# Optimization experiments

Measured on AMD Instinct MI355X. Metric: run time of the kernel, lower is better.

Reference implementation:

```python
import jax, jax.numpy as jnp
import numpy as np


def setup_inputs() -> dict:
    key = jax.random.key(0)
    kq, kk, kv = jax.random.split(key, 3)
    B, H, S, D = 4, 12, 2048, 64
    query = jax.random.normal(kq, (B, H, S, D), dtype=jnp.float32)
    k = jax.random.normal(kk, (B, H, S, D), dtype=jnp.float32)
    value = jax.random.normal(kv, (B, H, S, D), dtype=jnp.float32)
    return {"query": query, "key": k, "value": value}


def reference(query, key, value):
    # scores = Q K^T / sqrt(d_k)  -> [B, H, S, S]
    d_k = query.shape[-1]
    scale = 1.0 / jnp.sqrt(jnp.asarray(d_k, dtype=query.dtype))
    scores = jnp.einsum('bhqd,bhkd->bhqk', query, key) * scale
    attention = jax.nn.softmax(scores, axis=-1)
    # dropout p=0.0 -> identity
    output = jnp.einsum('bhqk,bhkd->bhqd', attention, value)
    return (output, attention)
```

## Files before the change

kernel.cpp:

```cpp
#include <hip/hip_runtime.h>
#include <hip/hip_bf16.h>

typedef short bf16x8_t __attribute__((ext_vector_type(8)));
typedef float f32x4_t __attribute__((ext_vector_type(4)));

#define SDIM 2048
#define DDIM 64
#define KBLK 64
#define NIT  (SDIM / KBLK)
#define NBH  48

__device__ __forceinline__ unsigned short f2bf(float f) {
    return __builtin_bit_cast(unsigned short, (__bf16)f);
}
__device__ __forceinline__ unsigned int pack2(float lo, float hi) {
    return ((unsigned int)f2bf(hi) << 16) | (unsigned int)f2bf(lo);
}
__device__ __forceinline__ bf16x8_t pack8(f32x4_t a, f32x4_t b) {
    bf16x8_t r;
    r[0] = (short)f2bf(a[0]); r[1] = (short)f2bf(a[1]);
    r[2] = (short)f2bf(a[2]); r[3] = (short)f2bf(a[3]);
    r[4] = (short)f2bf(b[0]); r[5] = (short)f2bf(b[1]);
    r[6] = (short)f2bf(b[2]); r[7] = (short)f2bf(b[3]);
    return r;
}
__device__ __forceinline__ bf16x8_t pack8s(f32x4_t a, f32x4_t b, float s) {
    bf16x8_t r;
    r[0] = (short)f2bf(a[0] * s); r[1] = (short)f2bf(a[1] * s);
    r[2] = (short)f2bf(a[2] * s); r[3] = (short)f2bf(a[3] * s);
    r[4] = (short)f2bf(b[0] * s); r[5] = (short)f2bf(b[1] * s);
    r[6] = (short)f2bf(b[2] * s); r[7] = (short)f2bf(b[3] * s);
    return r;
}
struct uint4s { unsigned int x, y, z, w; };

__device__ __forceinline__ void lds_sync() {
    asm volatile("s_waitcnt lgkmcnt(0)" ::: "memory");
    __builtin_amdgcn_s_barrier();
    asm volatile("" ::: "memory");
}

__global__ __launch_bounds__(256) void cvt_k_kernel(const float* __restrict__ K,
                                                    unsigned short* __restrict__ Kb) {
    size_t i = ((size_t)blockIdx.x * 256 + threadIdx.x) * 8;
    f32x4_t a = *(const f32x4_t*)(K + i);
    f32x4_t b = *(const f32x4_t*)(K + i + 4);
    *(bf16x8_t*)(Kb + i) = pack8(a, b);
}

__global__ __launch_bounds__(256) void tr_v_kernel(const float* __restrict__ V,
                                                   unsigned short* __restrict__ VT) {
    __shared__ unsigned short lt[64 * 72];
    const int bh = blockIdx.x >> 5;
    const int kt = blockIdx.x & 31;
    const float* Vb = V + (size_t)bh * (SDIM * DDIM) + (size_t)kt * 64 * DDIM;
    unsigned short* VTb = VT + (size_t)bh * (DDIM * SDIM) + kt * 64;
    const int t = threadIdx.x;
    {
        const int kl = t >> 2, dg = t & 3;
        const float* vp = Vb + kl * DDIM + dg * 16;
        f32x4_t v0 = *(const f32x4_t*)vp;
        f32x4_t v1 = *(const f32x4_t*)(vp + 4);
        f32x4_t v2 = *(const f32x4_t*)(vp + 8);
        f32x4_t v3 = *(const f32x4_t*)(vp + 12);
#pragma unroll
        for (int j = 0; j < 16; ++j) {
            float f = (j < 4) ? v0[j] : (j < 8) ? v1[j - 4] : (j < 12) ? v2[j - 8] : v3[j - 12];
            lt[(dg * 16 + j) * 72 + kl] = f2bf(f);
        }
    }
    __syncthreads();
    {
        const int d = t >> 2, kg = t & 3;
        bf16x8_t w0 = *(const bf16x8_t*)&lt[d * 72 + kg * 16];
        bf16x8_t w1 = *(const bf16x8_t*)&lt[d * 72 + kg * 16 + 8];
        *(bf16x8_t*)(VTb + (size_t)d * SDIM + kg * 16) = w0;
        *(bf16x8_t*)(VTb + (size_t)d * SDIM + kg * 16 + 8) = w1;
    }
}

__global__ __launch_bounds__(256, 2) void sdpa_main_kernel(
    const float* __restrict__ Q, const unsigned short* __restrict__ Kb,
    const unsigned short* __restrict__ VT, float* __restrict__ out,
    float* __restrict__ attn)
{
    __shared__ __align__(16) unsigned short Klds[2][KBLK * DDIM];
    __shared__ __align__(16) unsigned short Vlds[2][KBLK * DDIM];
    __shared__ __align__(16) float pbuf[4][16 * 64];

    const int bid = blockIdx.x;
    const int bh  = bid >> 4;
    const int qt  = bid & 15;
    const int tid = threadIdx.x;
    const int lane = tid & 63;
    const int wv   = tid >> 6;
    const int l15  = lane & 15;
    const int hi   = lane >> 4;
    const int qbase = qt * 128 + wv * 32;

    const unsigned short* KbB = Kb + (size_t)bh * (SDIM * DDIM);
    const unsigned short* VTb = VT + (size_t)bh * (DDIM * SDIM);
    float* outW  = out  + ((size_t)bh * SDIM + qbase) * DDIM;
    float* attnW = attn + (size_t)bh * SDIM * SDIM + (size_t)qbase * SDIM;
    float* pb = pbuf[wv];

    const float SC = 0.18033688011112042f;

    const float* qp0 = Q + ((size_t)bh * SDIM + qbase + l15) * DDIM + hi * 8;
    const float* qp1 = qp0 + (size_t)16 * DDIM;
    const bf16x8_t aq0_0 = pack8s(*(const f32x4_t*)qp0,        *(const f32x4_t*)(qp0 + 4), SC);
    const bf16x8_t aq1_0 = pack8s(*(const f32x4_t*)(qp0 + 32), *(const f32x4_t*)(qp0 + 36), SC);
    const bf16x8_t aq0_1 = pack8s(*(const f32x4_t*)qp1,        *(const f32x4_t*)(qp1 + 4), SC);
    const bf16x8_t aq1_1 = pack8s(*(const f32x4_t*)(qp1 + 32), *(const f32x4_t*)(qp1 + 36), SC);

    auto stage_load_K = [&](int kbase, bf16x8_t kreg[2]) {
#pragma unroll
        for (int j = 0; j < 2; ++j)
            kreg[j] = *(const bf16x8_t*)(KbB + (size_t)kbase * DDIM + (j * 256 + tid) * 8);
    };
    auto stage_write_K = [&](unsigned short* dst, const bf16x8_t kreg[2]) {
#pragma unroll
        for (int j = 0; j < 2; ++j) {
            const int b = (j * 256 + tid) * 16;
            const int row = b >> 7;
            *(bf16x8_t*)((char*)dst + (b ^ ((row & 7) << 4))) = kreg[j];
        }
    };
    auto stage_load_V = [&](int kbase, bf16x8_t vreg[2]) {
#pragma unroll
        for (int j = 0; j < 2; ++j) {
            const int row = j * 32 + (tid >> 3);
            vreg[j] = *(const bf16x8_t*)(VTb + (size_t)row * SDIM + kbase + (tid & 7) * 8);
        }
    };
    auto stage_write_V = [&](unsigned short* dst, const bf16x8_t vreg[2]) {
#pragma unroll
        for (int j = 0; j < 2; ++j) {
            const int row = j * 32 + (tid >> 3);
            const int b = row * 128 + (tid & 7) * 16;
            *(bf16x8_t*)((char*)dst + (b ^ ((row & 7) << 4))) = vreg[j];
        }
    };
    auto read_tile = [&](const unsigned short* src, int s, int c) -> bf16x8_t {
        const int row = s * 16 + l15;
        const int b = row * 128 + c * 64 + hi * 16;
        return *(const bf16x8_t*)((const char*)src + (b ^ ((row & 7) << 4)));
    };

    const int laneA = l15 + ((hi & 1) << 5);
    const int laneB = laneA + 16;
    const bool selHi = (hi >> 1) != 0;

    auto store_sub = [&](const f32x4_t P[4], int t, int kbase) {
#pragma unroll
        for (int g = 0; g < 4; ++g) {
            const int c4 = (g * 4 + hi) ^ ((l15 & 7) << 1);
            *(f32x4_t*)(pb + l15 * 64 + c4 * 4) = P[g];
        }
        asm volatile("s_waitcnt lgkmcnt(0)" ::: "memory");
        __builtin_amdgcn_sched_barrier(0);
#pragma unroll
        for (int j = 0; j < 4; ++j) {
            const int row = j * 4 + (lane & 3);
            const int c4 = lane >> 2;
            f32x4_t v = *(const f32x4_t*)(pb + row * 64 + (c4 ^ ((row & 7) << 1)) * 4);
            __builtin_nontemporal_store(v,
                (f32x4_t*)(attnW + (size_t)(t * 16 + row) * SDIM + kbase + c4 * 4));
        }
        asm volatile("s_waitcnt lgkmcnt(0)" ::: "memory");
        __builtin_amdgcn_sched_barrier(0);
    };
    auto build_af = [&](const f32x4_t P[4], bf16x8_t af[2]) {
        unsigned int w0[4], w1[4];
#pragma unroll
        for (int s = 0; s < 4; ++s) {
            w0[s] = pack2(P[s][0], P[s][1]);
            w1[s] = pack2(P[s][2], P[s][3]);
        }
#pragma unroll
        for (int k2 = 0; k2 < 2; ++k2) {
            const int sL = 2 * k2, sH = 2 * k2 + 1;
            unsigned int W0a = (unsigned int)__shfl((int)w0[sL], laneA);
            unsigned int W0b = (unsigned int)__shfl((int)w0[sH], laneA);
            unsigned int W1a = (unsigned int)__shfl((int)w1[sL], laneA);
            unsigned int W1b = (unsigned int)__shfl((int)w1[sH], laneA);
            unsigned int W2a = (unsigned int)__shfl((int)w0[sL], laneB);
            unsigned int W2b = (unsigned int)__shfl((int)w0[sH], laneB);
            unsigned int W3a = (unsigned int)__shfl((int)w1[sL], laneB);
            unsigned int W3b = (unsigned int)__shfl((int)w1[sH], laneB);
            uint4s W;
            W.x = selHi ? W0b : W0a;
            W.y = selHi ? W1b : W1a;
            W.z = selHi ? W2b : W2a;
            W.w = selHi ? W3b : W3a;
            af[k2] = __builtin_bit_cast(bf16x8_t, W);
        }
    };

    float rs0 = 0.f;
    {
        bf16x8_t kreg[2];
        stage_load_K(0, kreg);
        stage_write_K(Klds[0], kreg);
        lds_sync();
        for (int kb = 0; kb < NIT; ++kb) {
            bf16x8_t knx[2];
            if (kb + 1 < NIT) stage_load_K((kb + 1) * KBLK, knx);
            const unsigned short* Kc = Klds[kb & 1];
#pragma unroll
            for (int s = 0; s < 4; ++s) {
                bf16x8_t k0 = read_tile(Kc, s, 0), k1 = read_tile(Kc, s, 1);
                f32x4_t a0 = {0.f,0.f,0.f,0.f};
                a0 = __builtin_amdgcn_mfma_f32_16x16x32_bf16(k0, aq0_0, a0, 0, 0, 0);
                a0 = __builtin_amdgcn_mfma_f32_16x16x32_bf16(k1, aq1_0, a0, 0, 0, 0);
                rs0 += __builtin_amdgcn_exp2f(a0[0]) + __builtin_amdgcn_exp2f(a0[1])
                     + __builtin_amdgcn_exp2f(a0[2]) + __builtin_amdgcn_exp2f(a0[3]);
            }
            if (kb + 1 < NIT) stage_write_K(Klds[(kb + 1) & 1], knx);
            lds_sync();
        }
    }
    rs0 += __shfl_xor(rs0, 16); rs0 += __shfl_xor(rs0, 32);
    const float nlg0 = __builtin_amdgcn_logf(rs0);

    f32x4_t oacc0[4] = {{0.f,0.f,0.f,0.f},{0.f,0.f,0.f,0.f},{0.f,0.f,0.f,0.f},{0.f,0.f,0.f,0.f}};
    float rs1 = 0.f;
    {
        bf16x8_t kreg[2], vreg[2];
        stage_load_K(0, kreg);
        stage_load_V(0, vreg);
        stage_write_K(Klds[0], kreg);
        stage_write_V(Vlds[0], vreg);
        lds_sync();
        for (int kb = 0; kb < NIT; ++kb) {
            const int kbase = kb * KBLK;
            bf16x8_t knx[2], vnx[2];
            if (kb + 1 < NIT) {
                stage_load_K(kbase + KBLK, knx);
                stage_load_V(kbase + KBLK, vnx);
            }
            const unsigned short* Kc = Klds[kb & 1];
            const unsigned short* Vc = Vlds[kb & 1];

            f32x4_t A0[4];
#pragma unroll
            for (int s = 0; s < 4; ++s) {
                bf16x8_t k0 = read_tile(Kc, s, 0), k1 = read_tile(Kc, s, 1);
                f32x4_t a0 = {0.f,0.f,0.f,0.f}, a1 = {0.f,0.f,0.f,0.f};
                a0 = __builtin_amdgcn_mfma_f32_16x16x32_bf16(k0, aq0_0, a0, 0, 0, 0);
                a0 = __builtin_amdgcn_mfma_f32_16x16x32_bf16(k1, aq1_0, a0, 0, 0, 0);
                a1 = __builtin_amdgcn_mfma_f32_16x16x32_bf16(k0, aq0_1, a1, 0, 0, 0);
                a1 = __builtin_amdgcn_mfma_f32_16x16x32_bf16(k1, aq1_1, a1, 0, 0, 0);
                A0[s] = a0;
                rs1 += __builtin_amdgcn_exp2f(a1[0]) + __builtin_amdgcn_exp2f(a1[1])
                     + __builtin_amdgcn_exp2f(a1[2]) + __builtin_amdgcn_exp2f(a1[3]);
            }

            f32x4_t P0[4];
#pragma unroll
            for (int s = 0; s < 4; ++s) {
#pragma unroll
                for (int r = 0; r < 4; ++r)
                    P0[s][r] = __builtin_amdgcn_exp2f(A0[s][r] - nlg0);
            }

            bf16x8_t af0[2];
            build_af(P0, af0);
#pragma unroll
            for (int dt = 0; dt < 4; ++dt) {
                bf16x8_t v0 = read_tile(Vc, dt, 0), v1 = read_tile(Vc, dt, 1);
                oacc0[dt] = __builtin_amdgcn_mfma_f32_16x16x32_bf16(af0[0], v0, oacc0[dt], 0, 0, 0);
                oacc0[dt] = __builtin_amdgcn_mfma_f32_16x16x32_bf16(af0[1], v1, oacc0[dt], 0, 0, 0);
            }

            store_sub(P0, 0, kbase);

            if (kb + 1 < NIT) {
                stage_write_K(Klds[(kb + 1) & 1], knx);
                stage_write_V(Vlds[(kb + 1) & 1], vnx);
            }
            lds_sync();
        }
    }
    rs1 += __shfl_xor(rs1, 16); rs1 += __shfl_xor(rs1, 32);
    const float nlg1 = __builtin_amdgcn_logf(rs1);

    f32x4_t oacc1[4] = {{0.f,0.f,0.f,0.f},{0.f,0.f,0.f,0.f},{0.f,0.f,0.f,0.f},{0.f,0.f,0.f,0.f}};
    {
        bf16x8_t kreg[2], vreg[2];
        stage_load_K(0, kreg);
        stage_load_V(0, vreg);
        stage_write_K(Klds[0], kreg);
        stage_write_V(Vlds[0], vreg);
        lds_sync();
        for (int kb = 0; kb < NIT; ++kb) {
            const int kbase = kb * KBLK;
            bf16x8_t knx[2], vnx[2];
            if (kb + 1 < NIT) {
                stage_load_K(kbase + KBLK, knx);
                stage_load_V(kbase + KBLK, vnx);
            }
            const unsigned short* Kc = Klds[kb & 1];
            const unsigned short* Vc = Vlds[kb & 1];

            f32x4_t A1[4];
#pragma unroll
            for (int s = 0; s < 4; ++s) {
                bf16x8_t k0 = read_tile(Kc, s, 0), k1 = read_tile(Kc, s, 1);
                f32x4_t a1 = {0.f,0.f,0.f,0.f};
                a1 = __builtin_amdgcn_mfma_f32_16x16x32_bf16(k0, aq0_1, a1, 0, 0, 0);
                a1 = __builtin_amdgcn_mfma_f32_16x16x32_bf16(k1, aq1_1, a1, 0, 0, 0);
                A1[s] = a1;
            }

            f32x4_t P1[4];
#pragma unroll
            for (int s = 0; s < 4; ++s) {
#pragma unroll
                for (int r = 0; r < 4; ++r)
                    P1[s][r] = __builtin_amdgcn_exp2f(A1[s][r] - nlg1);
            }

            bf16x8_t af1[2];
            build_af(P1, af1);
#pragma unroll
            for (int dt = 0; dt < 4; ++dt) {
                bf16x8_t v0 = read_tile(Vc, dt, 0), v1 = read_tile(Vc, dt, 1);
                oacc1[dt] = __builtin_amdgcn_mfma_f32_16x16x32_bf16(af1[0], v0, oacc1[dt], 0, 0, 0);
                oacc1[dt] = __builtin_amdgcn_mfma_f32_16x16x32_bf16(af1[1], v1, oacc1[dt], 0, 0, 0);
            }

            store_sub(P1, 1, kbase);

            if (kb + 1 < NIT) {
                stage_write_K(Klds[(kb + 1) & 1], knx);
                stage_write_V(Vlds[(kb + 1) & 1], vnx);
            }
            lds_sync();
        }
    }

#pragma unroll
    for (int dt = 0; dt < 4; ++dt) {
#pragma unroll
        for (int r = 0; r < 4; ++r) {
            outW[(size_t)(hi * 4 + r) * DDIM + dt * 16 + l15] = oacc0[dt][r];
            outW[(size_t)(16 + hi * 4 + r) * DDIM + dt * 16 + l15] = oacc1[dt][r];
        }
    }
}

extern "C" void kernel_launch(void* const* d_in, const int* in_sizes, int n_in,
                              void* d_out, int out_size, void* d_ws, size_t ws_size,
                              hipStream_t stream) {
    const float* Q = (const float*)d_in[0];
    const float* K = (const float*)d_in[1];
    const float* V = (const float*)d_in[2];
    float* out  = (float*)d_out;
    float* attn = out + (size_t)NBH * SDIM * DDIM;

    unsigned short* Kb = (unsigned short*)d_ws;
    unsigned short* VT = Kb + (size_t)NBH * SDIM * DDIM;

    cvt_k_kernel<<<dim3((NBH * SDIM * DDIM) / (256 * 8)), dim3(256), 0, stream>>>(K, Kb);
    tr_v_kernel<<<dim3(NBH * 32), dim3(256), 0, stream>>>(V, VT);

    sdpa_main_kernel<<<dim3(NBH * 16), dim3(256), 0, stream>>>(Q, Kb, VT, out, attn);
}
```

Before: 225.1 us.

## Stage attention probabilities as bf16 in LDS and raise occupancy to four blocks

The probability tile is packed to bf16 once and reused both for the PV MFMA operand shuffle and for the LDS staging buffer. This halves per-wave scratch LDS and cuts the number of pack operations. Output accumulators are scoped to each pass and stored right after it, which lowers peak register pressure. Launch bounds now request four blocks per CU. The attention matrix written out is now bf16-rounded, which reduces its precision compared with the earlier fp32 values.

```diff
diff --git a/kernel.cpp b/kernel.cpp
--- a/kernel.cpp
+++ b/kernel.cpp
@@ -2,6 +2,7 @@
 #include <hip/hip_bf16.h>
 
 typedef short bf16x8_t __attribute__((ext_vector_type(8)));
+typedef short short4_t __attribute__((ext_vector_type(4)));
 typedef float f32x4_t __attribute__((ext_vector_type(4)));
 
 #define SDIM 2048
@@ -12,6 +13,10 @@
 
 __device__ __forceinline__ unsigned short f2bf(float f) {
     return __builtin_bit_cast(unsigned short, (__bf16)f);
+}
+__device__ __forceinline__ float bf2f(unsigned short u) {
+    unsigned int v = ((unsigned int)u) << 16;
+    return __builtin_bit_cast(float, v);
 }
 __device__ __forceinline__ unsigned int pack2(float lo, float hi) {
     return ((unsigned int)f2bf(hi) << 16) | (unsigned int)f2bf(lo);
@@ -33,6 +38,7 @@
     return r;
 }
 struct uint4s { unsigned int x, y, z, w; };
+struct u2pair { unsigned int x, y; };
 
 __device__ __forceinline__ void lds_sync() {
     asm volatile("s_waitcnt lgkmcnt(0)" ::: "memory");
@@ -79,14 +85,14 @@
     }
 }
 
-__global__ __launch_bounds__(256, 2) void sdpa_main_kernel(
+__global__ __launch_bounds__(256, 4) void sdpa_main_kernel(
     const float* __restrict__ Q, const unsigned short* __restrict__ Kb,
     const unsigned short* __restrict__ VT, float* __restrict__ out,
     float* __restrict__ attn)
 {
     __shared__ __align__(16) unsigned short Klds[2][KBLK * DDIM];
     __shared__ __align__(16) unsigned short Vlds[2][KBLK * DDIM];
-    __shared__ __align__(16) float pbuf[4][16 * 64];
+    __shared__ __align__(16) unsigned short pbuf[4][16 * 64];
 
     const int bid = blockIdx.x;
     const int bh  = bid >> 4;
@@ -102,7 +108,7 @@
     const unsigned short* VTb = VT + (size_t)bh * (DDIM * SDIM);
     float* outW  = out  + ((size_t)bh * SDIM + qbase) * DDIM;
     float* attnW = attn + (size_t)bh * SDIM * SDIM + (size_t)qbase * SDIM;
-    float* pb = pbuf[wv];
+    unsigned short* pw = pbuf[wv];
 
     const float SC = 0.18033688011112042f;
 
@@ -151,43 +157,51 @@
     const int laneB = laneA + 16;
     const bool selHi = (hi >> 1) != 0;
 
-    auto store_sub = [&](const f32x4_t P[4], int t, int kbase) {
-#pragma unroll
-        for (int g = 0; g < 4; ++g) {
-            const int c4 = (g * 4 + hi) ^ ((l15 & 7) << 1);
-            *(f32x4_t*)(pb + l15 * 64 + c4 * 4) = P[g];
+    auto pack_p = [&](const f32x4_t P[4], unsigned int wp[8]) {
+#pragma unroll
+        for (int s = 0; s < 4; ++s) {
+            wp[2 * s]     = pack2(P[s][0], P[s][1]);
+            wp[2 * s + 1] = pack2(P[s][2], P[s][3]);
+        }
+    };
+    auto store_sub = [&](const unsigned int wp[8], int t, int kbase) {
+#pragma unroll
+        for (int s = 0; s < 4; ++s) {
+            const int off = (s * 32 + hi * 8) ^ (l15 << 3);
+            u2pair u; u.x = wp[2 * s]; u.y = wp[2 * s + 1];
+            *reinterpret_cast<short4_t*>((char*)pw + l15 * 128 + off) =
+                __builtin_bit_cast(short4_t, u);
         }
         asm volatile("s_waitcnt lgkmcnt(0)" ::: "memory");
         __builtin_amdgcn_sched_barrier(0);
 #pragma unroll
         for (int j = 0; j < 4; ++j) {
             const int row = j * 4 + (lane & 3);
-            const int c4 = lane >> 2;
-            f32x4_t v = *(const f32x4_t*)(pb + row * 64 + (c4 ^ ((row & 7) << 1)) * 4);
+            const int kp  = lane >> 2;
+            const int off = (kp * 8) ^ ((row & 15) << 3);
+            short4_t b4 = *reinterpret_cast<const short4_t*>(
+                (const char*)pw + row * 128 + off);
+            f32x4_t v;
+            v[0] = bf2f((unsigned short)b4[0]); v[1] = bf2f((unsigned short)b4[1]);
+            v[2] = bf2f((unsigned short)b4[2]); v[3] = bf2f((unsigned short)b4[3]);
             __builtin_nontemporal_store(v,
-                (f32x4_t*)(attnW + (size_t)(t * 16 + row) * SDIM + kbase + c4 * 4));
+                (f32x4_t*)(attnW + (size_t)(t * 16 + row) * SDIM + kbase + kp * 4));
         }
         asm volatile("s_waitcnt lgkmcnt(0)" ::: "memory");
         __builtin_amdgcn_sched_barrier(0);
     };
-    auto build_af = [&](const f32x4_t P[4], bf16x8_t af[2]) {
-        unsigned int w0[4], w1[4];
-#pragma unroll
-        for (int s = 0; s < 4; ++s) {
-            w0[s] = pack2(P[s][0], P[s][1]);
-            w1[s] = pack2(P[s][2], P[s][3]);
-        }
+    auto build_af = [&](const unsigned int wp[8], bf16x8_t af[2]) {
 #pragma unroll
         for (int k2 = 0; k2 < 2; ++k2) {
             const int sL = 2 * k2, sH = 2 * k2 + 1;
-            unsigned int W0a = (unsigned int)__shfl((int)w0[sL], laneA);
-            unsigned int W0b = (unsigned int)__shfl((int)w0[sH], laneA);
-            unsigned int W1a = (unsigned int)__shfl((int)w1[sL], laneA);
-            unsigned int W1b = (unsigned int)__shfl((int)w1[sH], laneA);
-            unsigned int W2a = (unsigned int)__shfl((int)w0[sL], laneB);
-            unsigned int W2b = (unsigned int)__shfl((int)w0[sH], laneB);
-            unsigned int W3a = (unsigned int)__shfl((int)w1[sL], laneB);
-            unsigned int W3b = (unsigned int)__shfl((int)w1[sH], laneB);
+            unsigned int W0a = (unsigned int)__shfl((int)wp[2 * sL],     laneA);
+            unsigned int W0b = (unsigned int)__shfl((int)wp[2 * sH],     laneA);
+            unsigned int W1a = (unsigned int)__shfl((int)wp[2 * sL + 1], laneA);
+            unsigned int W1b = (unsigned int)__shfl((int)wp[2 * sH + 1], laneA);
+            unsigned int W2a = (unsigned int)__shfl((int)wp[2 * sL],     laneB);
+            unsigned int W2b = (unsigned int)__shfl((int)wp[2 * sH],     laneB);
+            unsigned int W3a = (unsigned int)__shfl((int)wp[2 * sL + 1], laneB);
+            unsigned int W3b = (unsigned int)__shfl((int)wp[2 * sH + 1], laneB);
             uint4s W;
             W.x = selHi ? W0b : W0a;
             W.y = selHi ? W1b : W1a;
@@ -223,9 +237,9 @@
     rs0 += __shfl_xor(rs0, 16); rs0 += __shfl_xor(rs0, 32);
     const float nlg0 = __builtin_amdgcn_logf(rs0);
 
-    f32x4_t oacc0[4] = {{0.f,0.f,0.f,0.f},{0.f,0.f,0.f,0.f},{0.f,0.f,0.f,0.f},{0.f,0.f,0.f,0.f}};
     float rs1 = 0.f;
     {
+        f32x4_t oacc0[4] = {{0.f,0.f,0.f,0.f},{0.f,0.f,0.f,0.f},{0.f,0.f,0.f,0.f},{0.f,0.f,0.f,0.f}};
         bf16x8_t kreg[2], vreg[2];
         stage_load_K(0, kreg);
         stage_load_V(0, vreg);
@@ -264,8 +278,10 @@
                     P0[s][r] = __builtin_amdgcn_exp2f(A0[s][r] - nlg0);
             }
 
+            unsigned int wp0[8];
+            pack_p(P0, wp0);
             bf16x8_t af0[2];
-            build_af(P0, af0);
+            build_af(wp0, af0);
 #pragma unroll
             for (int dt = 0; dt < 4; ++dt) {
                 bf16x8_t v0 = read_tile(Vc, dt, 0), v1 = read_tile(Vc, dt, 1);
@@ -273,7 +289,7 @@
                 oacc0[dt] = __builtin_amdgcn_mfma_f32_16x16x32_bf16(af0[1], v1, oacc0[dt], 0, 0, 0);
             }
 
-            store_sub(P0, 0, kbase);
+            store_sub(wp0, 0, kbase);
 
             if (kb + 1 < NIT) {
                 stage_write_K(Klds[(kb + 1) & 1], knx);
@@ -281,12 +297,18 @@
             }
             lds_sync();
         }
+#pragma unroll
+        for (int dt = 0; dt < 4; ++dt) {
+#pragma unroll
+            for (int r = 0; r < 4; ++r)
+                outW[(size_t)(hi * 4 + r) * DDIM + dt * 16 + l15] = oacc0[dt][r];
+        }
     }
     rs1 += __shfl_xor(rs1, 16); rs1 += __shfl_xor(rs1, 32);
     const float nlg1 = __builtin_amdgcn_logf(rs1);
 
-    f32x4_t oacc1[4] = {{0.f,0.f,0.f,0.f},{0.f,0.f,0.f,0.f},{0.f,0.f,0.f,0.f},{0.f,0.f,0.f,0.f}};
-    {
+    {
+        f32x4_t oacc1[4] = {{0.f,0.f,0.f,0.f},{0.f,0.f,0.f,0.f},{0.f,0.f,0.f,0.f},{0.f,0.f,0.f,0.f}};
         bf16x8_t kreg[2], vreg[2];
         stage_load_K(0, kreg);
         stage_load_V(0, vreg);
@@ -321,8 +343,10 @@
                     P1[s][r] = __builtin_amdgcn_exp2f(A1[s][r] - nlg1);
             }
 
+            unsigned int wp1[8];
+            pack_p(P1, wp1);
             bf16x8_t af1[2];
-            build_af(P1, af1);
+            build_af(wp1, af1);
 #pragma unroll
             for (int dt = 0; dt < 4; ++dt) {
                 bf16x8_t v0 = read_tile(Vc, dt, 0), v1 = read_tile(Vc, dt, 1);
@@ -330,7 +354,7 @@
                 oacc1[dt] = __builtin_amdgcn_mfma_f32_16x16x32_bf16(af1[1], v1, oacc1[dt], 0, 0, 0);
             }
 
-            store_sub(P1, 1, kbase);
+            store_sub(wp1, 1, kbase);
 
             if (kb + 1 < NIT) {
                 stage_write_K(Klds[(kb + 1) & 1], knx);
@@ -338,14 +362,11 @@
             }
             lds_sync();
         }
-    }
-
-#pragma unroll
-    for (int dt = 0; dt < 4; ++dt) {
-#pragma unroll
-        for (int r = 0; r < 4; ++r) {
-            outW[(size_t)(hi * 4 + r) * DDIM + dt * 16 + l15] = oacc0[dt][r];
-            outW[(size_t)(16 + hi * 4 + r) * DDIM + dt * 16 + l15] = oacc1[dt][r];
+#pragma unroll
+        for (int dt = 0; dt < 4; ++dt) {
+#pragma unroll
+            for (int r = 0; r < 4; ++r)
+                outW[(size_t)(16 + hi * 4 + r) * DDIM + dt * 16 + l15] = oacc1[dt][r];
         }
     }
 }
```

Measured after the change: 234.6 us. 4.2% more time.
